# Performance work log

Hardware: AMD Instinct MI355X
Metric: run time of the kernel (lower is better)

Reference implementation:

```python
import jax, jax.numpy as jnp
import numpy as np

NEG_SLOPE_GAT = 0.2   # PyG GATConv default negative_slope
NEG_SLOPE_OUT = 0.01  # F.leaky_relu default in GAT_Layer.forward
HEADS = 1

def setup_inputs() -> dict:
    key = jax.random.key(0)
    ks = jax.random.split(key, 6)
    N, E, V, D = 100000, 1600000, 50000, 64
    x = jax.random.randint(ks[0], (N,), 0, V, dtype=jnp.int64)
    edge_index = jax.random.randint(ks[1], (2, E), 0, N, dtype=jnp.int64)
    emb_table = jax.random.normal(ks[2], (V, D), dtype=jnp.float32)
    W = jax.random.normal(ks[3], (D, HEADS * D), dtype=jnp.float32) / jnp.sqrt(D).astype(jnp.float32)
    att_src = jax.random.normal(ks[4], (HEADS, D), dtype=jnp.float32)
    att_dst = jax.random.normal(ks[5], (HEADS, D), dtype=jnp.float32)
    bias = jnp.zeros((HEADS * D,), dtype=jnp.float32)
    return {"x": x, "edge_index": edge_index, "emb_table": emb_table,
            "W": W, "att_src": att_src, "att_dst": att_dst, "bias": bias}

def reference(x, edge_index, emb_table, W, att_src, att_dst, bias):
    N = x.shape[0]
    H = HEADS
    # embedding lookup
    x_embed = emb_table[x]                                # [N, D]
    # PyG GATConv adds self-loops by default
    loops = jnp.arange(N, dtype=edge_index.dtype)
    src = jnp.concatenate([edge_index[0], loops])         # [E+N]
    dst = jnp.concatenate([edge_index[1], loops])         # [E+N]
    # linear projection -> per-head features
    h = (x_embed @ W).reshape(N, H, -1)                   # [N, H, C]
    # per-node attention logits
    a_src = jnp.sum(h * att_src[None], axis=-1)           # [N, H]
    a_dst = jnp.sum(h * att_dst[None], axis=-1)           # [N, H]
    # per-edge score (gather)
    e = jax.nn.leaky_relu(a_src[src] + a_dst[dst], NEG_SLOPE_GAT)  # [E+N, H]
    # segment softmax over incoming edges of each dst node
    m = jax.ops.segment_max(e, dst, num_segments=N)       # every node has a self-loop
    ex = jnp.exp(e - m[dst])
    s = jax.ops.segment_sum(ex, dst, num_segments=N)
    alpha = ex / (s[dst] + 1e-16)                          # [E+N, H]
    # weighted scatter-aggregate of source messages
    msg = h[src] * alpha[:, :, None]                       # [E+N, H, C]
    x_gat = jax.ops.segment_sum(msg, dst, num_segments=N).reshape(N, -1) + bias
    # GAT_Layer.forward: out = leaky_relu(x_gat); dropout is identity in eval
    out = jax.nn.leaky_relu(x_gat, NEG_SLOPE_OUT)
    return out, alpha
```

## Files before the change

kernel.cpp:

```cpp
#include <hip/hip_runtime.h>
#include <hip/hip_bf16.h>
#include <math.h>

#define D 64
#define NEG_GAT 0.2f
#define NEG_OUT 0.01f
#define CHUNK 256
#define MAXD 256
#define BSH 8
#define NBMAX 512
#define PART_K 16
#define NODE_BLOCKS 2048

typedef __hip_bfloat16 bf16;

__device__ __forceinline__ float bf_lo(unsigned u) { return __uint_as_float(u << 16); }
__device__ __forceinline__ float bf_hi(unsigned u) { return __uint_as_float(u & 0xffff0000u); }

__global__ void k_init(int* __restrict__ rp, int N) {
    int n = blockIdx.x * blockDim.x + threadIdx.x;
    if (n < N) rp[n] = 1;
}

__global__ void k_count(const int* __restrict__ dstI, int* __restrict__ rp, int E) {
    int i = blockIdx.x * blockDim.x + threadIdx.x;
    if (i < E) atomicAdd(&rp[dstI[i]], 1);
}

__global__ void k_scan1(const int* __restrict__ rp, int* __restrict__ partial, int N) {
    __shared__ int sm[CHUNK];
    int n = blockIdx.x * CHUNK + threadIdx.x;
    sm[threadIdx.x] = (n < N) ? rp[n] : 0;
    __syncthreads();
    for (int off = CHUNK / 2; off > 0; off >>= 1) {
        if (threadIdx.x < off) sm[threadIdx.x] += sm[threadIdx.x + off];
        __syncthreads();
    }
    if (threadIdx.x == 0) partial[blockIdx.x] = sm[0];
}

__global__ void k_scan2(int* __restrict__ partial, int NC) {
    __shared__ int sm[512];
    int t = threadIdx.x;
    int v = (t < NC) ? partial[t] : 0;
    sm[t] = v;
    __syncthreads();
    for (int off = 1; off < 512; off <<= 1) {
        int xv = (t >= off) ? sm[t - off] : 0;
        __syncthreads();
        sm[t] += xv;
        __syncthreads();
    }
    if (t < NC) partial[t] = sm[t] - v;
}

__global__ void k_scan3(int* __restrict__ rp, const int* __restrict__ partial, int N) {
    __shared__ int sm[CHUNK];
    int b = blockIdx.x, t = threadIdx.x;
    int n = b * CHUNK + t;
    int v = (n < N) ? rp[n] : 0;
    sm[t] = v;
    __syncthreads();
    for (int off = 1; off < CHUNK; off <<= 1) {
        int xv = (t >= off) ? sm[t - off] : 0;
        __syncthreads();
        sm[t] += xv;
        __syncthreads();
    }
    if (n < N) rp[n] = partial[b] + sm[t] - v;
}

__global__ void k_place(const int* __restrict__ srcI, const int* __restrict__ dstI,
                        int* __restrict__ rp, int* __restrict__ perm, int E, int N) {
    int i = blockIdx.x * blockDim.x + threadIdx.x;
    if (i >= E + N) return;
    int dn, sn;
    if (i < E) { dn = dstI[i]; sn = srcI[i]; }
    else       { dn = i - E;   sn = dn; }
    int pos = atomicAdd(&rp[dn], 1);
    perm[pos] = sn;
}

__global__ void k_bzero(int* __restrict__ bh, int NB1) {
    int t = blockIdx.x * blockDim.x + threadIdx.x;
    if (t < NB1) bh[t] = 0;
}

__global__ void k_bhist(const int* __restrict__ dstI, int* __restrict__ bh,
                        int E, int N) {
    __shared__ int lh[NBMAX];
    for (int t = threadIdx.x; t < NBMAX; t += blockDim.x) lh[t] = 0;
    __syncthreads();
    const int EN = E + N;
    for (int i = blockIdx.x * blockDim.x + threadIdx.x; i < EN;
         i += gridDim.x * blockDim.x) {
        int dn = (i < E) ? dstI[i] : (i - E);
        atomicAdd(&lh[dn >> BSH], 1);
    }
    __syncthreads();
    for (int t = threadIdx.x; t < NBMAX; t += blockDim.x)
        if (lh[t]) atomicAdd(&bh[t], lh[t]);
}

__global__ void k_bscan(int* __restrict__ bh, int* __restrict__ bcur, int NB) {
    __shared__ int sm[NBMAX];
    int t = threadIdx.x;
    int v = (t < NB) ? bh[t] : 0;
    sm[t] = v;
    __syncthreads();
    for (int off = 1; off < NBMAX; off <<= 1) {
        int xv = (t >= off) ? sm[t - off] : 0;
        __syncthreads();
        sm[t] += xv;
        __syncthreads();
    }
    if (t < NB) { int st = sm[t] - v; bh[t] = st; bcur[t] = st; }
}

__global__ void k_part(const int* __restrict__ srcI, const int* __restrict__ dstI,
                       int* __restrict__ bcur, unsigned* __restrict__ staging,
                       int E, int N) {
    __shared__ int lh[NBMAX];
    __shared__ int gb[NBMAX];
    const int EN = E + N;
    const int tid = threadIdx.x;
    const long long base = (long long)blockIdx.x * (256 * PART_K);

    for (int t = tid; t < NBMAX; t += 256) lh[t] = 0;
    __syncthreads();

    int bb[PART_K], rr[PART_K];
#pragma unroll
    for (int k = 0; k < PART_K; ++k) {
        long long i = base + (long long)k * 256 + tid;
        bb[k] = -1; rr[k] = 0;
        if (i < EN) {
            int dn = (i < E) ? dstI[i] : (int)(i - E);
            bb[k] = dn >> BSH;
            rr[k] = atomicAdd(&lh[bb[k]], 1);
        }
    }
    __syncthreads();
    for (int t = tid; t < NBMAX; t += 256) {
        int c = lh[t];
        gb[t] = c ? atomicAdd(&bcur[t], c) : 0;
    }
    __syncthreads();
#pragma unroll
    for (int k = 0; k < PART_K; ++k) {
        if (bb[k] >= 0) {
            long long i = base + (long long)k * 256 + tid;
            int dn, sn;
            if (i < E) { dn = dstI[i]; sn = srcI[i]; }
            else       { dn = (int)(i - E); sn = dn; }
            staging[(long long)gb[bb[k]] + rr[k]] =
                ((unsigned)sn << BSH) | (unsigned)(dn & ((1 << BSH) - 1));
        }
    }
}

__global__ void k_place3(const unsigned* __restrict__ staging,
                         const int* __restrict__ bstart, const int* __restrict__ bend,
                         int* __restrict__ rp, int* __restrict__ perm, int N) {
    __shared__ int cnt[256];
    __shared__ int scan[256];
    const int b = blockIdx.x;
    const int t = threadIdx.x;
    const int nbase = b << BSH;
    const int s = bstart[b], e = bend[b];

    cnt[t] = 0;
    __syncthreads();
    for (int j = s + t; j < e; j += 256)
        atomicAdd(&cnt[staging[j] & ((1 << BSH) - 1)], 1);
    __syncthreads();
    int v = cnt[t];
    scan[t] = v;
    __syncthreads();
    for (int off = 1; off < 256; off <<= 1) {
        int y = (t >= off) ? scan[t - off] : 0;
        __syncthreads();
        scan[t] += y;
        __syncthreads();
    }
    const int incl = scan[t];
    const int excl = incl - v;
    const int n = nbase + t;
    if (n < N) rp[n] = s + incl;
    __syncthreads();
    scan[t] = excl;
    __syncthreads();
    for (int j = s + t; j < e; j += 256) {
        unsigned pk = staging[j];
        int loc = pk & ((1 << BSH) - 1);
        int pos = s + atomicAdd(&scan[loc], 1);
        perm[pos] = (int)(pk >> BSH);
    }
}

__global__ void __launch_bounds__(256)
k_node(const int* __restrict__ x,
       const float* __restrict__ emb,
       const float* __restrict__ W,
       const float* __restrict__ att_src,
       const float* __restrict__ att_dst,
       bf16* __restrict__ hb,
       float* __restrict__ a_src, float* __restrict__ a_dst,
       int N)
{
    __shared__ float Wl[D * D];
    for (int i = threadIdx.x; i < D * D; i += blockDim.x) Wl[i] = W[i];
    __syncthreads();

    const int lane = threadIdx.x & 63;
    const int wave = threadIdx.x >> 6;

    float wreg[D];
#pragma unroll
    for (int d = 0; d < D; ++d) wreg[d] = Wl[d * D + lane];

    const float asl = att_src[lane];
    const float adl = att_dst[lane];
    const int stride = gridDim.x * 4;

    int n = blockIdx.x * 4 + wave;
    for (; n + stride < N; n += 2 * stride) {
        const int n2 = n + stride;
        const int xa = __builtin_amdgcn_readfirstlane(x[n]);
        const int xb = __builtin_amdgcn_readfirstlane(x[n2]);
        const float* ea = emb + (long long)xa * D;
        const float* eb = emb + (long long)xb * D;

        float h1 = 0.0f, h2 = 0.0f;
#pragma unroll
        for (int d = 0; d < D; ++d) {
            h1 = fmaf(ea[d], wreg[d], h1);
            h2 = fmaf(eb[d], wreg[d], h2);
        }
        hb[(long long)n  * D + lane] = __float2bfloat16(h1);
        hb[(long long)n2 * D + lane] = __float2bfloat16(h2);

        float vs1 = h1 * asl, vd1 = h1 * adl;
        float vs2 = h2 * asl, vd2 = h2 * adl;
#pragma unroll
        for (int o = 32; o >= 1; o >>= 1) {
            vs1 += __shfl_xor(vs1, o);
            vd1 += __shfl_xor(vd1, o);
            vs2 += __shfl_xor(vs2, o);
            vd2 += __shfl_xor(vd2, o);
        }
        if (lane == 0) {
            a_src[n]  = vs1; a_dst[n]  = vd1;
            a_src[n2] = vs2; a_dst[n2] = vd2;
        }
    }
    for (; n < N; n += stride) {
        const int xn = __builtin_amdgcn_readfirstlane(x[n]);
        const float* er = emb + (long long)xn * D;
        float hc = 0.0f;
#pragma unroll
        for (int d = 0; d < D; ++d)
            hc = fmaf(er[d], wreg[d], hc);
        hb[(long long)n * D + lane] = __float2bfloat16(hc);
        float vs = hc * asl, vd = hc * adl;
#pragma unroll
        for (int o = 32; o >= 1; o >>= 1) {
            vs += __shfl_xor(vs, o);
            vd += __shfl_xor(vd, o);
        }
        if (lane == 0) { a_src[n] = vs; a_dst[n] = vd; }
    }
}

__global__ void k_agg(const int* __restrict__ rp,
                      const int* __restrict__ perm,
                      const float* __restrict__ a_src,
                      const float* __restrict__ a_dst,
                      const bf16* __restrict__ hb,
                      const float* __restrict__ bias,
                      float* __restrict__ out,
                      float* __restrict__ scale_ws,
                      int E, int N)
{
    __shared__ int   sn_s[4][MAXD];
    __shared__ float al_s[4][MAXD];

    const int lane = threadIdx.x & 63;
    const int w    = threadIdx.x >> 6;
    const int n = blockIdx.x * 4 + w;
    if (n >= N) return;

    const int base = (n == 0) ? 0 : rp[n - 1];
    const int deg  = rp[n] - base;
    const float adn = a_dst[n];

    if (deg <= MAXD) {
        float mx = -1e30f;
        for (int j = lane; j < deg; j += 64) {
            int sn = perm[base + j];
            sn_s[w][j] = sn;
            float lg = a_src[sn] + adn;
            lg = lg > 0.0f ? lg : NEG_GAT * lg;
            al_s[w][j] = lg;
            mx = fmaxf(mx, lg);
        }
#pragma unroll
        for (int o = 32; o >= 1; o >>= 1) mx = fmaxf(mx, __shfl_xor(mx, o));

        float se = 0.0f;
        for (int j = lane; j < deg; j += 64) {
            float ex = __expf(al_s[w][j] - mx);
            al_s[w][j] = ex;
            se += ex;
        }
#pragma unroll
        for (int o = 32; o >= 1; o >>= 1) se += __shfl_xor(se, o);
        const float inv = 1.0f / (se + 1e-16f);
        if (lane == 0) scale_ws[n] = inv * __expf(-mx);

        const int e = lane >> 3;
        const int c = lane & 7;
        float acc[8] = {0.f, 0.f, 0.f, 0.f, 0.f, 0.f, 0.f, 0.f};
#pragma unroll 4
        for (int j = e; j < deg; j += 8) {
            const float al = al_s[w][j];
            const uint4 u =
                reinterpret_cast<const uint4*>(hb + (long long)sn_s[w][j] * D)[c];
            acc[0] = fmaf(al, bf_lo(u.x), acc[0]);
            acc[1] = fmaf(al, bf_hi(u.x), acc[1]);
            acc[2] = fmaf(al, bf_lo(u.y), acc[2]);
            acc[3] = fmaf(al, bf_hi(u.y), acc[3]);
            acc[4] = fmaf(al, bf_lo(u.z), acc[4]);
            acc[5] = fmaf(al, bf_hi(u.z), acc[5]);
            acc[6] = fmaf(al, bf_lo(u.w), acc[6]);
            acc[7] = fmaf(al, bf_hi(u.w), acc[7]);
        }
#pragma unroll
        for (int o = 8; o <= 32; o <<= 1) {
#pragma unroll
            for (int k = 0; k < 8; ++k) acc[k] += __shfl_xor(acc[k], o);
        }

        if (lane < 8) {
            const float4 b0 = reinterpret_cast<const float4*>(bias)[2 * c];
            const float4 b1 = reinterpret_cast<const float4*>(bias)[2 * c + 1];
            float4 v0, v1;
            v0.x = acc[0] * inv + b0.x;
            v0.y = acc[1] * inv + b0.y;
            v0.z = acc[2] * inv + b0.z;
            v0.w = acc[3] * inv + b0.w;
            v1.x = acc[4] * inv + b1.x;
            v1.y = acc[5] * inv + b1.y;
            v1.z = acc[6] * inv + b1.z;
            v1.w = acc[7] * inv + b1.w;
            v0.x = v0.x > 0.0f ? v0.x : NEG_OUT * v0.x;
            v0.y = v0.y > 0.0f ? v0.y : NEG_OUT * v0.y;
            v0.z = v0.z > 0.0f ? v0.z : NEG_OUT * v0.z;
            v0.w = v0.w > 0.0f ? v0.w : NEG_OUT * v0.w;
            v1.x = v1.x > 0.0f ? v1.x : NEG_OUT * v1.x;
            v1.y = v1.y > 0.0f ? v1.y : NEG_OUT * v1.y;
            v1.z = v1.z > 0.0f ? v1.z : NEG_OUT * v1.z;
            v1.w = v1.w > 0.0f ? v1.w : NEG_OUT * v1.w;
            float4* orow = reinterpret_cast<float4*>(out + (long long)n * D);
            orow[2 * c]     = v0;
            orow[2 * c + 1] = v1;
        }
    } else {
        float mx = -1e30f;
        for (int j = lane; j < deg; j += 64) {
            int sn = perm[base + j];
            float lg = a_src[sn] + adn;
            lg = lg > 0.0f ? lg : NEG_GAT * lg;
            mx = fmaxf(mx, lg);
        }
#pragma unroll
        for (int o = 32; o >= 1; o >>= 1) mx = fmaxf(mx, __shfl_xor(mx, o));

        float se = 0.0f;
        for (int j = lane; j < deg; j += 64) {
            int sn = perm[base + j];
            float lg = a_src[sn] + adn;
            lg = lg > 0.0f ? lg : NEG_GAT * lg;
            se += __expf(lg - mx);
        }
#pragma unroll
        for (int o = 32; o >= 1; o >>= 1) se += __shfl_xor(se, o);
        const float inv = 1.0f / (se + 1e-16f);
        if (lane == 0) scale_ws[n] = inv * __expf(-mx);

        float acc = 0.0f;
        for (int j = 0; j < deg; ++j) {
            int sn = perm[base + j];
            float lg = a_src[sn] + adn;
            lg = lg > 0.0f ? lg : NEG_GAT * lg;
            float al = __expf(lg - mx) * inv;
            acc = fmaf(al, __bfloat162float(hb[(long long)sn * D + lane]), acc);
        }
        float v = acc + bias[lane];
        v = v > 0.0f ? v : NEG_OUT * v;
        out[(long long)n * D + lane] = v;
    }
}

__global__ void k_alpha(const int* __restrict__ srcI, const int* __restrict__ dstI,
                        const float* __restrict__ a_src, const float* __restrict__ a_dst,
                        const float* __restrict__ scale_ws,
                        float* __restrict__ alpha_out, int E, int N)
{
    int i = blockIdx.x * blockDim.x + threadIdx.x;
    if (i >= E + N) return;
    int sn, dn;
    if (i < E) { sn = srcI[i]; dn = dstI[i]; }
    else       { sn = dn = i - E; }
    float lg = a_src[sn] + a_dst[dn];
    lg = lg > 0.0f ? lg : NEG_GAT * lg;
    alpha_out[i] = __expf(lg) * scale_ws[dn];
}

extern "C" void kernel_launch(void* const* d_in, const int* in_sizes, int n_in,
                              void* d_out, int out_size, void* d_ws, size_t ws_size,
                              hipStream_t stream)
{
    const int* x          = (const int*)d_in[0];
    const int* ei         = (const int*)d_in[1];
    const float* emb      = (const float*)d_in[2];
    const float* W        = (const float*)d_in[3];
    const float* att_src  = (const float*)d_in[4];
    const float* att_dst  = (const float*)d_in[5];
    const float* bias     = (const float*)d_in[6];

    const int N = in_sizes[0];
    const int E = in_sizes[1] / 2;
    const int* srcI = ei;
    const int* dstI = ei + E;
    const int NC = (N + CHUNK - 1) / CHUNK;
    const int NB = (N + (1 << BSH) - 1) >> BSH;
    const int EN = E + N;

    char* p = (char*)d_ws;
    size_t off = 0;
    auto take = [&](size_t bytes) {
        char* q = p + off;
        off += (bytes + 15) & ~size_t(15);
        return q;
    };
    int* partial      = (int*)take((size_t)NC * 4);
    int* rp           = (int*)take((size_t)N * 4);
    float* a_src_b    = (float*)take((size_t)N * 4);
    float* a_dst_b    = (float*)take((size_t)N * 4);
    float* scale_ws   = (float*)take((size_t)N * 4);
    int* perm         = (int*)take((size_t)EN * 4);
    int* bh           = (int*)take((size_t)(NBMAX + 1) * 4);
    int* bcur         = (int*)take((size_t)NBMAX * 4);
    unsigned* staging = (unsigned*)take((size_t)EN * 4);
    bf16* hb          = (bf16*)take((size_t)N * D * 2);

    float* out       = (float*)d_out;
    float* alpha_out = out + (long long)N * D;

    const bool bucketed = (NB <= NBMAX) && (N < (1 << 23));
    const int node_grid = min(NODE_BLOCKS, (N + 3) / 4);

    k_node  <<<node_grid, 256, 0, stream>>>(x, emb, W, att_src, att_dst,
                                            hb, a_src_b, a_dst_b, N);
    if (bucketed) {
        k_bzero <<<(NBMAX + 256) / 256, 256, 0, stream>>>(bh, NBMAX + 1);
        k_bhist <<<512, 256, 0, stream>>>(dstI, bh, E, N);
        k_bscan <<<1, NBMAX, 0, stream>>>(bh, bcur, NB);
        k_part  <<<(EN + 256 * PART_K - 1) / (256 * PART_K), 256, 0, stream>>>(
                    srcI, dstI, bcur, staging, E, N);
        k_place3<<<NB, 256, 0, stream>>>(staging, bh, bcur, rp, perm, N);
    } else {
        k_init  <<<(N + 255) / 256, 256, 0, stream>>>(rp, N);
        k_count <<<(E + 255) / 256, 256, 0, stream>>>(dstI, rp, E);
        k_scan1 <<<NC, CHUNK, 0, stream>>>(rp, partial, N);
        k_scan2 <<<1, 512, 0, stream>>>(partial, NC);
        k_scan3 <<<NC, CHUNK, 0, stream>>>(rp, partial, N);
        k_place <<<(EN + 255) / 256, 256, 0, stream>>>(srcI, dstI, rp, perm, E, N);
    }
    k_agg  <<<(N + 3) / 4, 256, 0, stream>>>(rp, perm, a_src_b, a_dst_b,
                                             hb, bias, out, scale_ws, E, N);
    k_alpha<<<(EN + 255) / 256, 256, 0, stream>>>(srcI, dstI, a_src_b, a_dst_b,
                                                  scale_ws, alpha_out, E, N);
}
```

Measured before the change: 196.1 us.

## Vectorize alpha kernel, unroll projection to four nodes, reduce agg unroll

Adds a k_alpha4 kernel in which each thread handles four edges, using int4 loads of src/dst indices and a float4 store of alpha, and launches it when E is a multiple of four. The projection kernel now processes four nodes per wave iteration instead of two, giving more independent embedding loads in flight. The aggregation gather loop's unroll drops from 4 to 2, likely to lower register pressure. The wider unroll in the projection raises register use and may cut occupancy.

```diff
diff --git a/kernel.cpp b/kernel.cpp
--- a/kernel.cpp
+++ b/kernel.cpp
@@ -224,34 +224,46 @@
     const int stride = gridDim.x * 4;
 
     int n = blockIdx.x * 4 + wave;
-    for (; n + stride < N; n += 2 * stride) {
-        const int n2 = n + stride;
-        const int xa = __builtin_amdgcn_readfirstlane(x[n]);
-        const int xb = __builtin_amdgcn_readfirstlane(x[n2]);
+    for (; n + 3 * stride < N; n += 4 * stride) {
+        const int na = n, nb2 = n + stride, nc = n + 2 * stride, nd = n + 3 * stride;
+        const int xa = __builtin_amdgcn_readfirstlane(x[na]);
+        const int xb = __builtin_amdgcn_readfirstlane(x[nb2]);
+        const int xc = __builtin_amdgcn_readfirstlane(x[nc]);
+        const int xd = __builtin_amdgcn_readfirstlane(x[nd]);
         const float* ea = emb + (long long)xa * D;
         const float* eb = emb + (long long)xb * D;
-
-        float h1 = 0.0f, h2 = 0.0f;
+        const float* ec = emb + (long long)xc * D;
+        const float* ed = emb + (long long)xd * D;
+
+        float h1 = 0.0f, h2 = 0.0f, h3 = 0.0f, h4 = 0.0f;
 #pragma unroll
         for (int d = 0; d < D; ++d) {
             h1 = fmaf(ea[d], wreg[d], h1);
             h2 = fmaf(eb[d], wreg[d], h2);
-        }
-        hb[(long long)n  * D + lane] = __float2bfloat16(h1);
-        hb[(long long)n2 * D + lane] = __float2bfloat16(h2);
+            h3 = fmaf(ec[d], wreg[d], h3);
+            h4 = fmaf(ed[d], wreg[d], h4);
+        }
+        hb[(long long)na  * D + lane] = __float2bfloat16(h1);
+        hb[(long long)nb2 * D + lane] = __float2bfloat16(h2);
+        hb[(long long)nc  * D + lane] = __float2bfloat16(h3);
+        hb[(long long)nd  * D + lane] = __float2bfloat16(h4);
 
         float vs1 = h1 * asl, vd1 = h1 * adl;
         float vs2 = h2 * asl, vd2 = h2 * adl;
+        float vs3 = h3 * asl, vd3 = h3 * adl;
+        float vs4 = h4 * asl, vd4 = h4 * adl;
 #pragma unroll
         for (int o = 32; o >= 1; o >>= 1) {
-            vs1 += __shfl_xor(vs1, o);
-            vd1 += __shfl_xor(vd1, o);
-            vs2 += __shfl_xor(vs2, o);
-            vd2 += __shfl_xor(vd2, o);
+            vs1 += __shfl_xor(vs1, o);  vd1 += __shfl_xor(vd1, o);
+            vs2 += __shfl_xor(vs2, o);  vd2 += __shfl_xor(vd2, o);
+            vs3 += __shfl_xor(vs3, o);  vd3 += __shfl_xor(vd3, o);
+            vs4 += __shfl_xor(vs4, o);  vd4 += __shfl_xor(vd4, o);
         }
         if (lane == 0) {
-            a_src[n]  = vs1; a_dst[n]  = vd1;
-            a_src[n2] = vs2; a_dst[n2] = vd2;
+            a_src[na]  = vs1; a_dst[na]  = vd1;
+            a_src[nb2] = vs2; a_dst[nb2] = vd2;
+            a_src[nc]  = vs3; a_dst[nc]  = vd3;
+            a_src[nd]  = vs4; a_dst[nd]  = vd4;
         }
     }
     for (; n < N; n += stride) {
@@ -321,7 +333,7 @@
         const int e = lane >> 3;
         const int c = lane & 7;
         float acc[8] = {0.f, 0.f, 0.f, 0.f, 0.f, 0.f, 0.f, 0.f};
-#pragma unroll 4
+#pragma unroll 2
         for (int j = e; j < deg; j += 8) {
             const float al = al_s[w][j];
             const uint4 u =
@@ -402,6 +414,54 @@
     }
 }
 
+__global__ void k_alpha4(const int* __restrict__ srcI, const int* __restrict__ dstI,
+                         const float* __restrict__ a_src, const float* __restrict__ a_dst,
+                         const float* __restrict__ scale_ws,
+                         float* __restrict__ alpha_out, int E, int N)
+{
+    const int i4 = (blockIdx.x * blockDim.x + threadIdx.x) * 4;
+    const int EN = E + N;
+    if (i4 >= EN) return;
+    if (i4 + 3 < E) {
+        const int4 s4 = *reinterpret_cast<const int4*>(srcI + i4);
+        const int4 d4 = *reinterpret_cast<const int4*>(dstI + i4);
+        float4 r;
+        {
+            float lg = a_src[s4.x] + a_dst[d4.x];
+            lg = lg > 0.0f ? lg : NEG_GAT * lg;
+            r.x = __expf(lg) * scale_ws[d4.x];
+        }
+        {
+            float lg = a_src[s4.y] + a_dst[d4.y];
+            lg = lg > 0.0f ? lg : NEG_GAT * lg;
+            r.y = __expf(lg) * scale_ws[d4.y];
+        }
+        {
+            float lg = a_src[s4.z] + a_dst[d4.z];
+            lg = lg > 0.0f ? lg : NEG_GAT * lg;
+            r.z = __expf(lg) * scale_ws[d4.z];
+        }
+        {
+            float lg = a_src[s4.w] + a_dst[d4.w];
+            lg = lg > 0.0f ? lg : NEG_GAT * lg;
+            r.w = __expf(lg) * scale_ws[d4.w];
+        }
+        *reinterpret_cast<float4*>(alpha_out + i4) = r;
+    } else {
+#pragma unroll
+        for (int k = 0; k < 4; ++k) {
+            int i = i4 + k;
+            if (i >= EN) break;
+            int sn, dn;
+            if (i < E) { sn = srcI[i]; dn = dstI[i]; }
+            else       { sn = dn = i - E; }
+            float lg = a_src[sn] + a_dst[dn];
+            lg = lg > 0.0f ? lg : NEG_GAT * lg;
+            alpha_out[i] = __expf(lg) * scale_ws[dn];
+        }
+    }
+}
+
 __global__ void k_alpha(const int* __restrict__ srcI, const int* __restrict__ dstI,
                         const float* __restrict__ a_src, const float* __restrict__ a_dst,
                         const float* __restrict__ scale_ws,
@@ -480,6 +540,11 @@
     }
     k_agg  <<<(N + 3) / 4, 256, 0, stream>>>(rp, perm, a_src_b, a_dst_b,
                                              hb, bias, out, scale_ws, E, N);
-    k_alpha<<<(EN + 255) / 256, 256, 0, stream>>>(srcI, dstI, a_src_b, a_dst_b,
-                                                  scale_ws, alpha_out, E, N);
-}
+    if ((E & 3) == 0) {
+        k_alpha4<<<((EN + 3) / 4 + 255) / 256, 256, 0, stream>>>(
+                    srcI, dstI, a_src_b, a_dst_b, scale_ws, alpha_out, E, N);
+    } else {
+        k_alpha <<<(EN + 255) / 256, 256, 0, stream>>>(
+                    srcI, dstI, a_src_b, a_dst_b, scale_ws, alpha_out, E, N);
+    }
+}
```

After: 196.9 us. No clear change (+0.4%).
